# Performance work log

Measured on AMD Instinct MI355X. Metric: run time of the kernel, lower is better.

The kernel has to match this reference:

```python
import jax, jax.numpy as jnp
import numpy as np

B, T, NEMBD, NVOCAB, HID = 32, 64, 64, 256, 4096


def setup_inputs() -> dict:
    key = jax.random.key(0)
    ks = jax.random.split(key, 12)
    s = 0.1  # keep activations in a sane range
    return {
        "X": jax.random.randint(ks[0], (B, T), 0, NVOCAB, dtype=jnp.int32),
        "M": jnp.ones((B, T, 1), dtype=jnp.float32),
        "S": jnp.zeros((2, B, HID), dtype=jnp.float32),
        "embd": jax.random.normal(ks[1], (NVOCAB, NEMBD), jnp.float32) * s,
        "wx": jax.random.normal(ks[2], (NEMBD, 4 * HID), jnp.float32) * s,
        "wh": jax.random.normal(ks[3], (HID, 4 * HID), jnp.float32) * s,
        "wmx": jax.random.normal(ks[4], (NEMBD, HID), jnp.float32) * s,
        "wmh": jax.random.normal(ks[5], (HID, HID), jnp.float32) * s,
        "b": jnp.zeros((4 * HID,), jnp.float32),
        "gx": jax.random.normal(ks[6], (4 * HID,), jnp.float32),
        "gh": jax.random.normal(ks[7], (4 * HID,), jnp.float32),
        "gmx": jax.random.normal(ks[8], (HID,), jnp.float32),
        "gmh": jax.random.normal(ks[9], (HID,), jnp.float32),
        "w_out": jax.random.normal(ks[10], (HID, NVOCAB), jnp.float32) * s,
        "b_out": jnp.zeros((NVOCAB,), jnp.float32),
    }


def _wn(w, g):
    # tf.nn.l2_normalize(w, dim=0) * g  (column-wise weight norm)
    return w * (g / jnp.sqrt(jnp.sum(w * w, axis=0, keepdims=True).clip(1e-12)))


def reference(X, M, S, embd, wx, wh, wmx, wmh, b, gx, gh, gmx, gmh, w_out, b_out):
    # weight-normalized rnn weights (rnn_wn=True)
    wxn, whn = _wn(wx, gx), _wn(wh, gh)
    wmxn, wmhn = _wn(wmx, gmx), _wn(wmh, gmh)

    words = embd[X]                       # [B,T,64]
    xs = jnp.swapaxes(words, 0, 1)        # [T,B,64]
    ms = jnp.swapaxes(M, 0, 1)            # [T,B,1]
    c0, h0 = S[0], S[1]                   # [B,HID] each

    def step(carry, inp):
        c, h = carry
        x, mt = inp
        m = (x @ wmxn) * (h @ wmhn)       # multiplicative intermediate
        z = x @ wxn + m @ whn + b         # [B,4*HID]
        i, f, o, u = jnp.split(z, 4, axis=1)
        i, f, o = jax.nn.sigmoid(i), jax.nn.sigmoid(f), jax.nn.sigmoid(o)
        u = jnp.tanh(u)
        ct = f * c + i * u
        ht = o * jnp.tanh(ct)
        c = ct * mt + c * (1.0 - mt)      # mask-blend state
        h = ht * mt + h * (1.0 - mt)
        return (c, h), (c, h)

    (cf, hf), (cells, hs) = jax.lax.scan(step, (c0, h0), (xs, ms))
    states = jnp.stack([cf, hf], 0)       # [2,B,HID]
    # tf.concat(hs,1) then reshape [-1,HID] => batch-major (b, t) row order
    hflat = jnp.swapaxes(hs, 0, 1).reshape(-1, hs.shape[-1])  # [B*T,HID]
    logits = hflat @ w_out + b_out        # out_wn=False
    return cells, states, logits
```

## Files before the change

### kernel.cpp

```cpp
#include <hip/hip_runtime.h>
#include <hip/hip_bf16.h>

#define HID 4096
#define NEMBD 64
#define NBATCH 32
#define NTIME 64
#define NVOCAB 256
#define G4 16384

typedef __attribute__((ext_vector_type(4))) float f32x4;
typedef __attribute__((ext_vector_type(8))) short s16x8;

__device__ __forceinline__ unsigned short f2bf(float f) {
  union { float f; unsigned u; } v; v.f = f;
  unsigned u = v.u + 0x7FFFu + ((v.u >> 16) & 1u);
  return (unsigned short)(u >> 16);
}

__device__ __forceinline__ int apoff(int b, int j) {
  return ((j >> 5) << 10) | ((b >> 4) << 9) |
         (((b & 15) | (((j >> 3) & 3) << 4)) << 3) | (j & 7);
}

__global__ void packs_k(const float* __restrict__ src, const float* __restrict__ g,
                        unsigned short* __restrict__ dst, float* __restrict__ sc,
                        int N, int Cw, int S, int nch) {
  int bid = blockIdx.x;
  int colbase = (bid & 3) * Cw + (bid >> S) * 16;
  size_t dstbase = (size_t)bid * nch * 512;
  __shared__ unsigned short tile[512];
  __shared__ float red[16][16];
  int tid = threadIdx.x;
  int col16 = tid & 15, kk = tid >> 4;
  float s = 0.f;
  for (int c = 0; c < nch; ++c) {
    float v0 = src[(size_t)(c * 32 + kk) * N + colbase + col16];
    float v1 = src[(size_t)(c * 32 + kk + 16) * N + colbase + col16];
    s += v0 * v0 + v1 * v1;
    int l0 = col16 | (((kk >> 3) & 3) << 4);
    int l1 = col16 | ((((kk + 16) >> 3) & 3) << 4);
    tile[l0 * 8 + (kk & 7)] = f2bf(v0);
    tile[l1 * 8 + (kk & 7)] = f2bf(v1);
    __syncthreads();
    if (tid < 64)
      ((s16x8*)(dst + dstbase + (size_t)c * 512))[tid] = ((s16x8*)tile)[tid];
    __syncthreads();
  }
  if (g) {
    red[kk][col16] = s;
    __syncthreads();
    if (tid < 16) {
      float tot = 0.f;
#pragma unroll
      for (int q = 0; q < 16; ++q) tot += red[q][tid];
      sc[colbase + tid] = g[colbase + tid] / sqrtf(fmaxf(tot, 1e-12f));
    }
  }
}

__global__ void xepack_k(const int* __restrict__ X, const float* __restrict__ embd,
                         unsigned short* __restrict__ xe) {
  int t = blockIdx.x;
  int tid = threadIdx.x;
  int l = tid & 63, tile = (tid >> 6) & 1, c2 = tid >> 7;
  int b = tile * 16 + (l & 15);
  int row = X[b * NTIME + t];
  int k0 = 32 * c2 + 8 * (l >> 4);
  size_t off = (size_t)t * 2048 + c2 * 1024 + tile * 512 + l * 8;
  for (int j = 0; j < 8; ++j) xe[off + j] = f2bf(embd[row * NEMBD + k0 + j]);
}

__global__ void init_k(const float* __restrict__ S, float* __restrict__ cst,
                       float* __restrict__ hst, unsigned short* __restrict__ hpk) {
  int e = blockIdx.x * 256 + threadIdx.x;
  if (e < NBATCH * HID) {
    float c = S[e], h = S[NBATCH * HID + e];
    cst[e] = c; hst[e] = h;
    int b = e >> 12, j = e & 4095;
    hpk[apoff(b, j)] = f2bf(h);
  }
}

#define MFMA(a, b, c) __builtin_amdgcn_mfma_f32_16x16x32_bf16(a, b, c, 0, 0, 0)

__global__ __launch_bounds__(1024, 4)
void ph1_k(const unsigned short* __restrict__ wmhp, const unsigned short* __restrict__ wmxp,
           const unsigned short* __restrict__ xe, const unsigned short* __restrict__ hpk,
           const float* __restrict__ scmh, const float* __restrict__ scmx,
           unsigned short* __restrict__ mpk, int t) {
  const int g = blockIdx.x;
  const int tid = threadIdx.x;
  const int w = tid >> 6, l = tid & 63;
  const int lo = l & 15, hi = l >> 4;

  __shared__ float part[16][32][16];
  __shared__ float xmS[32][16];

  const s16x8* wmh_g = (const s16x8*)(wmhp + (size_t)g * 128 * 512);
  const s16x8* wmx_g = (const s16x8*)(wmxp + (size_t)g * 2 * 512);
  const s16x8* hp = (const s16x8*)hpk;

  f32x4 a0 = {0.f, 0.f, 0.f, 0.f}, a1 = {0.f, 0.f, 0.f, 0.f};
  const int cb = w * 8;
  {
    s16x8 wbuf[4], pa[4], pb[4];
#pragma unroll
    for (int q = 0; q < 4; ++q) {
      wbuf[q] = wmh_g[(cb + q) * 64 + l];
      pa[q] = hp[(cb + q) * 128 + l];
      pb[q] = hp[(cb + q) * 128 + 64 + l];
    }
#pragma unroll
    for (int q = 0; q < 8; ++q) {
      const int r = q & 3;
      s16x8 bf = wbuf[r], af = pa[r], gf = pb[r];
      if (q < 4) {
        wbuf[r] = wmh_g[(cb + q + 4) * 64 + l];
        pa[r] = hp[(cb + q + 4) * 128 + l];
        pb[r] = hp[(cb + q + 4) * 128 + 64 + l];
      }
      a0 = MFMA(af, bf, a0);
      a1 = MFMA(gf, bf, a1);
    }
  }
#pragma unroll
  for (int r = 0; r < 4; ++r) {
    part[w][4 * hi + r][lo] = a0[r];
    part[w][16 + 4 * hi + r][lo] = a1[r];
  }
  if (w == 0) {
    f32x4 x0 = {0.f, 0.f, 0.f, 0.f}, x1 = {0.f, 0.f, 0.f, 0.f};
    const s16x8* xep = (const s16x8*)(xe + (size_t)t * 2048);
#pragma unroll
    for (int c2 = 0; c2 < 2; ++c2) {
      s16x8 bf = wmx_g[c2 * 64 + l];
      x0 = MFMA(xep[c2 * 128 + l], bf, x0);
      x1 = MFMA(xep[c2 * 128 + 64 + l], bf, x1);
    }
#pragma unroll
    for (int r = 0; r < 4; ++r) {
      xmS[4 * hi + r][lo] = x0[r];
      xmS[16 + 4 * hi + r][lo] = x1[r];
    }
  }
  __syncthreads();
  if (tid < 512) {
    const int eb = tid >> 4, c = tid & 15;
    const int ej = g * 16 + c;
    float hm = 0.f;
#pragma unroll
    for (int k = 0; k < 16; ++k) hm += part[k][eb][c];
    mpk[apoff(eb, ej)] = f2bf(xmS[eb][c] * hm * (scmh[ej] * scmx[ej]));
  }
}

__global__ __launch_bounds__(1024, 4)
void ph2_k(const unsigned short* __restrict__ whp, const unsigned short* __restrict__ wxp,
           const unsigned short* __restrict__ xe, const float* __restrict__ bias,
           const float* __restrict__ sch, const float* __restrict__ scx,
           const float* __restrict__ Mm, const unsigned short* __restrict__ mpk,
           unsigned short* __restrict__ hpk, float* __restrict__ cst,
           float* __restrict__ hst, unsigned short* __restrict__ hflat,
           float* __restrict__ out, int t) {
  const int g = blockIdx.x;
  const int tid = threadIdx.x;
  const int w = tid >> 6, l = tid & 63;
  const int lo = l & 15, hi = l >> 4;
  const int gate = w & 3, ks = w >> 2;

  __shared__ float part[16][32][16];
  __shared__ float xpart[4][32][16];

  const s16x8* wh_w = (const s16x8*)(whp + (size_t)(g * 4 + gate) * 128 * 512);
  const s16x8* wx_w = (const s16x8*)(wxp + (size_t)(g * 4 + gate) * 2 * 512);
  const s16x8* mp = (const s16x8*)mpk;

  f32x4 z0 = {0.f, 0.f, 0.f, 0.f}, z1 = {0.f, 0.f, 0.f, 0.f};
  const int cb = ks * 32;
  {
    s16x8 wbuf[4], pa[4], pb[4];
#pragma unroll
    for (int q = 0; q < 4; ++q) {
      wbuf[q] = wh_w[(cb + q) * 64 + l];
      pa[q] = mp[(cb + q) * 128 + l];
      pb[q] = mp[(cb + q) * 128 + 64 + l];
    }
#pragma unroll
    for (int q = 0; q < 32; ++q) {
      const int r = q & 3;
      s16x8 bf = wbuf[r], af = pa[r], gf = pb[r];
      if (q < 28) {
        wbuf[r] = wh_w[(cb + q + 4) * 64 + l];
        pa[r] = mp[(cb + q + 4) * 128 + l];
        pb[r] = mp[(cb + q + 4) * 128 + 64 + l];
      }
      z0 = MFMA(af, bf, z0);
      z1 = MFMA(gf, bf, z1);
    }
  }
  if (ks == 0) {
    f32x4 x0 = {0.f, 0.f, 0.f, 0.f}, x1 = {0.f, 0.f, 0.f, 0.f};
    const s16x8* xep = (const s16x8*)(xe + (size_t)t * 2048);
#pragma unroll
    for (int c2 = 0; c2 < 2; ++c2) {
      s16x8 bf = wx_w[c2 * 64 + l];
      x0 = MFMA(xep[c2 * 128 + l], bf, x0);
      x1 = MFMA(xep[c2 * 128 + 64 + l], bf, x1);
    }
#pragma unroll
    for (int r = 0; r < 4; ++r) {
      xpart[gate][4 * hi + r][lo] = x0[r];
      xpart[gate][16 + 4 * hi + r][lo] = x1[r];
    }
  }
#pragma unroll
  for (int r = 0; r < 4; ++r) {
    part[w][4 * hi + r][lo] = z0[r];
    part[w][16 + 4 * hi + r][lo] = z1[r];
  }
  __syncthreads();
  if (tid < 512) {
    const int eb = tid >> 4, c = tid & 15;
    const int ej = g * 16 + c;
    float zh, iv, fv, ov, uv;
    zh = part[0][eb][c] + part[4][eb][c] + part[8][eb][c] + part[12][eb][c];
    iv = zh * sch[ej] + xpart[0][eb][c] * scx[ej] + bias[ej];
    zh = part[1][eb][c] + part[5][eb][c] + part[9][eb][c] + part[13][eb][c];
    fv = zh * sch[4096 + ej] + xpart[1][eb][c] * scx[4096 + ej] + bias[4096 + ej];
    zh = part[2][eb][c] + part[6][eb][c] + part[10][eb][c] + part[14][eb][c];
    ov = zh * sch[8192 + ej] + xpart[2][eb][c] * scx[8192 + ej] + bias[8192 + ej];
    zh = part[3][eb][c] + part[7][eb][c] + part[11][eb][c] + part[15][eb][c];
    uv = zh * sch[12288 + ej] + xpart[3][eb][c] * scx[12288 + ej] + bias[12288 + ej];
    iv = 1.f / (1.f + __expf(-iv));
    fv = 1.f / (1.f + __expf(-fv));
    ov = 1.f / (1.f + __expf(-ov));
    uv = tanhf(uv);
    size_t sj = (size_t)eb * HID + ej;
    float cp = cst[sj], hpv = hst[sj];
    float ct = fv * cp + iv * uv;
    float ht = ov * tanhf(ct);
    float mt = Mm[eb * NTIME + t];
    float cn = ct * mt + cp * (1.f - mt);
    float hn = ht * mt + hpv * (1.f - mt);
    cst[sj] = cn;
    hst[sj] = hn;
    out[((size_t)t * NBATCH + eb) * HID + ej] = cn;
    unsigned short hb = f2bf(hn);
    {
      int tle = eb * 4 + (t >> 4);
      int r16 = t & 15;
      int kk2 = ej & 31;
      int lane2 = r16 | (((kk2 >> 3) & 3) << 4);
      hflat[(size_t)tle * 65536 + (size_t)(ej >> 5) * 512 + lane2 * 8 + (kk2 & 7)] = hb;
    }
    hpk[apoff(eb, ej)] = hb;
    if (t == NTIME - 1) {
      out[(size_t)NTIME * NBATCH * HID + sj] = cn;
      out[(size_t)NTIME * NBATCH * HID + NBATCH * HID + sj] = hn;
    }
  }
}

__global__ __launch_bounds__(256)
void logits_k(const unsigned short* __restrict__ hpA,
              const unsigned short* __restrict__ woutp,
              const float* __restrict__ bout, float* __restrict__ out) {
  int tle = blockIdx.x >> 1, ch = blockIdx.x & 1;
  int tid = threadIdx.x, w = tid >> 6, l = tid & 63;
  int lo = l & 15, hi = l >> 4;
  const s16x8* ap = (const s16x8*)(hpA + (size_t)tle * 65536);
  const s16x8* wp = (const s16x8*)woutp;
  f32x4 acc[2] = {{0.f,0.f,0.f,0.f},{0.f,0.f,0.f,0.f}};
  const int nt0 = ch * 8 + w * 2;
#pragma unroll 4
  for (int c = 0; c < 128; ++c) {
    s16x8 af = ap[c * 64 + l];
    acc[0] = MFMA(af, wp[((nt0 + 0) * 128 + c) * 64 + l], acc[0]);
    acc[1] = MFMA(af, wp[((nt0 + 1) * 128 + c) * 64 + l], acc[1]);
  }
  int r0 = tle * 16;
#pragma unroll
  for (int q = 0; q < 2; ++q) {
    int col = (nt0 + q) * 16 + lo;
    float bo = bout[col];
#pragma unroll
    for (int r = 0; r < 4; ++r)
      out[(size_t)(r0 + 4 * hi + r) * NVOCAB + col] = acc[q][r] + bo;
  }
}

extern "C" void kernel_launch(void* const* d_in, const int* in_sizes, int n_in,
                              void* d_out, int out_size, void* d_ws, size_t ws_size,
                              hipStream_t stream) {
  const int*   X    = (const int*)d_in[0];
  const float* Mm   = (const float*)d_in[1];
  const float* S    = (const float*)d_in[2];
  const float* embd = (const float*)d_in[3];
  const float* wx   = (const float*)d_in[4];
  const float* wh   = (const float*)d_in[5];
  const float* wmx  = (const float*)d_in[6];
  const float* wmh  = (const float*)d_in[7];
  const float* b    = (const float*)d_in[8];
  const float* gx   = (const float*)d_in[9];
  const float* gh   = (const float*)d_in[10];
  const float* gmx  = (const float*)d_in[11];
  const float* gmh  = (const float*)d_in[12];
  const float* wout = (const float*)d_in[13];
  const float* bout = (const float*)d_in[14];
  float* out = (float*)d_out;
  char* ws = (char*)d_ws;

  size_t cur = 0;
  auto alloc = [&](size_t bytes) { size_t o = cur; cur += (bytes + 255) & ~size_t(255); return o; };
  unsigned short* WHP   = (unsigned short*)(ws + alloc((size_t)1024 * 128 * 512 * 2));
  unsigned short* WMHP  = (unsigned short*)(ws + alloc((size_t)256 * 128 * 512 * 2));
  unsigned short* WXP   = (unsigned short*)(ws + alloc((size_t)1024 * 2 * 512 * 2));
  unsigned short* WMXP  = (unsigned short*)(ws + alloc((size_t)256 * 2 * 512 * 2));
  unsigned short* WOUTP = (unsigned short*)(ws + alloc((size_t)16 * 128 * 512 * 2));
  unsigned short* XE    = (unsigned short*)(ws + alloc((size_t)64 * 2048 * 2));
  unsigned short* MPK   = (unsigned short*)(ws + alloc((size_t)32 * 4096 * 2));
  unsigned short* HPK   = (unsigned short*)(ws + alloc((size_t)32 * 4096 * 2));
  float* CST            = (float*)(ws + alloc((size_t)32 * 4096 * 4));
  float* HST            = (float*)(ws + alloc((size_t)32 * 4096 * 4));
  unsigned short* HFLAT = (unsigned short*)(ws + alloc((size_t)2048 * 4096 * 2));
  float* SCH            = (float*)(ws + alloc((size_t)16384 * 4));
  float* SCX            = (float*)(ws + alloc((size_t)16384 * 4));
  float* SCMH           = (float*)(ws + alloc((size_t)4096 * 4));
  float* SCMX           = (float*)(ws + alloc((size_t)4096 * 4));
  (void)ws_size; (void)in_sizes; (void)n_in; (void)out_size;

  packs_k<<<1024, 256, 0, stream>>>(wh,   gh,  WHP,   SCH,  G4,    4096, 2, 128);
  packs_k<<<256,  256, 0, stream>>>(wmh,  gmh, WMHP,  SCMH, HID,   0,    0, 128);
  packs_k<<<1024, 256, 0, stream>>>(wx,   gx,  WXP,   SCX,  G4,    4096, 2, 2);
  packs_k<<<256,  256, 0, stream>>>(wmx,  gmx, WMXP,  SCMX, HID,   0,    0, 2);
  packs_k<<<16,   256, 0, stream>>>(wout, nullptr, WOUTP, nullptr, NVOCAB, 0, 0, 128);

  xepack_k<<<64, 256, 0, stream>>>(X, embd, XE);
  init_k<<<512, 256, 0, stream>>>(S, CST, HST, HPK);

  for (int t = 0; t < NTIME; ++t) {
    ph1_k<<<256, 1024, 0, stream>>>(WMHP, WMXP, XE, HPK, SCMH, SCMX, MPK, t);
    ph2_k<<<256, 1024, 0, stream>>>(WHP, WXP, XE, b, SCH, SCX, Mm, MPK, HPK, CST, HST,
                                    HFLAT, out, t);
  }

  logits_k<<<256, 256, 0, stream>>>(HFLAT, WOUTP, bout,
                                    out + (size_t)NTIME * NBATCH * HID + 2 * NBATCH * HID);
}
```

Measured before the change: 2.414 ms.

## Widen weight-pack reads to 64 columns and deepen weight prefetch in recurrent GEMMs

The weight packing kernel now has each block handle 64 contiguous columns, so every row read is a 256-byte coalesced access instead of 64 bytes, and fewer blocks are launched. In the per-timestep phase kernels, all eight weight fragments (ph1) or an 8-deep ring of them (ph2) are now prefetched, while the activation prefetch depth drops to 2. The goal is to hide more global-load latency on the large weight stream, at the cost of extra registers and possibly lower occupancy.

```diff
diff --git a/kernel.cpp b/kernel.cpp
--- a/kernel.cpp
+++ b/kernel.cpp
@@ -22,38 +22,39 @@
          (((b & 15) | (((j >> 3) & 3) << 4)) << 3) | (j & 7);
 }
 
-__global__ void packs_k(const float* __restrict__ src, const float* __restrict__ g,
-                        unsigned short* __restrict__ dst, float* __restrict__ sc,
-                        int N, int Cw, int S, int nch) {
-  int bid = blockIdx.x;
-  int colbase = (bid & 3) * Cw + (bid >> S) * 16;
-  size_t dstbase = (size_t)bid * nch * 512;
-  __shared__ unsigned short tile[512];
-  __shared__ float red[16][16];
-  int tid = threadIdx.x;
-  int col16 = tid & 15, kk = tid >> 4;
+__global__ void packs64_k(const float* __restrict__ src, const float* __restrict__ g,
+                          unsigned short* __restrict__ dst, float* __restrict__ sc,
+                          int N, int nch, int four) {
+  const int c0 = blockIdx.x * 64;
+  const int tid = threadIdx.x;
+  const int cl = tid & 63, kr = tid >> 6;
+  const int c = c0 + cl;
+  __shared__ unsigned short tile4[4][512];
+  __shared__ float red[4][64];
+  const int wti = tid >> 6;
+  const int wcol = c0 + wti * 16;
+  const int wtile = four ? ((((wcol & 4095) >> 4) << 2) | (wcol >> 12)) : (wcol >> 4);
+  unsigned short* wdst = dst + (size_t)wtile * nch * 512;
   float s = 0.f;
-  for (int c = 0; c < nch; ++c) {
-    float v0 = src[(size_t)(c * 32 + kk) * N + colbase + col16];
-    float v1 = src[(size_t)(c * 32 + kk + 16) * N + colbase + col16];
-    s += v0 * v0 + v1 * v1;
-    int l0 = col16 | (((kk >> 3) & 3) << 4);
-    int l1 = col16 | ((((kk + 16) >> 3) & 3) << 4);
-    tile[l0 * 8 + (kk & 7)] = f2bf(v0);
-    tile[l1 * 8 + (kk & 7)] = f2bf(v1);
+  const int ti = cl >> 4, col16 = cl & 15;
+  for (int ch = 0; ch < nch; ++ch) {
+#pragma unroll
+    for (int sub = 0; sub < 8; ++sub) {
+      int k32 = kr * 8 + sub;
+      float v = src[(size_t)(ch * 32 + k32) * N + c];
+      s += v * v;
+      tile4[ti][(col16 | (kr << 4)) * 8 + sub] = f2bf(v);
+    }
     __syncthreads();
-    if (tid < 64)
-      ((s16x8*)(dst + dstbase + (size_t)c * 512))[tid] = ((s16x8*)tile)[tid];
+    ((s16x8*)(wdst + (size_t)ch * 512))[tid & 63] = ((s16x8*)tile4[wti])[tid & 63];
     __syncthreads();
   }
   if (g) {
-    red[kk][col16] = s;
+    red[kr][cl] = s;
     __syncthreads();
-    if (tid < 16) {
-      float tot = 0.f;
-#pragma unroll
-      for (int q = 0; q < 16; ++q) tot += red[q][tid];
-      sc[colbase + tid] = g[colbase + tid] / sqrtf(fmaxf(tot, 1e-12f));
+    if (tid < 64) {
+      float tot = red[0][cl] + red[1][cl] + red[2][cl] + red[3][cl];
+      sc[c0 + cl] = g[c0 + cl] / sqrtf(fmaxf(tot, 1e-12f));
     }
   }
 }
@@ -103,21 +104,21 @@
   f32x4 a0 = {0.f, 0.f, 0.f, 0.f}, a1 = {0.f, 0.f, 0.f, 0.f};
   const int cb = w * 8;
   {
-    s16x8 wbuf[4], pa[4], pb[4];
-#pragma unroll
-    for (int q = 0; q < 4; ++q) {
-      wbuf[q] = wmh_g[(cb + q) * 64 + l];
+    s16x8 wbuf[8], pa[2], pb[2];
+#pragma unroll
+    for (int q = 0; q < 8; ++q) wbuf[q] = wmh_g[(cb + q) * 64 + l];
+#pragma unroll
+    for (int q = 0; q < 2; ++q) {
       pa[q] = hp[(cb + q) * 128 + l];
       pb[q] = hp[(cb + q) * 128 + 64 + l];
     }
 #pragma unroll
     for (int q = 0; q < 8; ++q) {
-      const int r = q & 3;
-      s16x8 bf = wbuf[r], af = pa[r], gf = pb[r];
-      if (q < 4) {
-        wbuf[r] = wmh_g[(cb + q + 4) * 64 + l];
-        pa[r] = hp[(cb + q + 4) * 128 + l];
-        pb[r] = hp[(cb + q + 4) * 128 + 64 + l];
+      const int r2 = q & 1;
+      s16x8 bf = wbuf[q], af = pa[r2], gf = pb[r2];
+      if (q < 6) {
+        pa[r2] = hp[(cb + q + 2) * 128 + l];
+        pb[r2] = hp[(cb + q + 2) * 128 + 64 + l];
       }
       a0 = MFMA(af, bf, a0);
       a1 = MFMA(gf, bf, a1);
@@ -178,21 +179,22 @@
   f32x4 z0 = {0.f, 0.f, 0.f, 0.f}, z1 = {0.f, 0.f, 0.f, 0.f};
   const int cb = ks * 32;
   {
-    s16x8 wbuf[4], pa[4], pb[4];
-#pragma unroll
-    for (int q = 0; q < 4; ++q) {
-      wbuf[q] = wh_w[(cb + q) * 64 + l];
+    s16x8 wbuf[8], pa[2], pb[2];
+#pragma unroll
+    for (int q = 0; q < 8; ++q) wbuf[q] = wh_w[(cb + q) * 64 + l];
+#pragma unroll
+    for (int q = 0; q < 2; ++q) {
       pa[q] = mp[(cb + q) * 128 + l];
       pb[q] = mp[(cb + q) * 128 + 64 + l];
     }
 #pragma unroll
     for (int q = 0; q < 32; ++q) {
-      const int r = q & 3;
-      s16x8 bf = wbuf[r], af = pa[r], gf = pb[r];
-      if (q < 28) {
-        wbuf[r] = wh_w[(cb + q + 4) * 64 + l];
-        pa[r] = mp[(cb + q + 4) * 128 + l];
-        pb[r] = mp[(cb + q + 4) * 128 + 64 + l];
+      const int r8 = q & 7, r2 = q & 1;
+      s16x8 bf = wbuf[r8], af = pa[r2], gf = pb[r2];
+      if (q < 24) wbuf[r8] = wh_w[(cb + q + 8) * 64 + l];
+      if (q < 30) {
+        pa[r2] = mp[(cb + q + 2) * 128 + l];
+        pb[r2] = mp[(cb + q + 2) * 128 + 64 + l];
       }
       z0 = MFMA(af, bf, z0);
       z1 = MFMA(gf, bf, z1);
@@ -329,11 +331,11 @@
   float* SCMX           = (float*)(ws + alloc((size_t)4096 * 4));
   (void)ws_size; (void)in_sizes; (void)n_in; (void)out_size;
 
-  packs_k<<<1024, 256, 0, stream>>>(wh,   gh,  WHP,   SCH,  G4,    4096, 2, 128);
-  packs_k<<<256,  256, 0, stream>>>(wmh,  gmh, WMHP,  SCMH, HID,   0,    0, 128);
-  packs_k<<<1024, 256, 0, stream>>>(wx,   gx,  WXP,   SCX,  G4,    4096, 2, 2);
-  packs_k<<<256,  256, 0, stream>>>(wmx,  gmx, WMXP,  SCMX, HID,   0,    0, 2);
-  packs_k<<<16,   256, 0, stream>>>(wout, nullptr, WOUTP, nullptr, NVOCAB, 0, 0, 128);
+  packs64_k<<<256, 256, 0, stream>>>(wh,   gh,  WHP,   SCH,  G4,    128, 1);
+  packs64_k<<<64,  256, 0, stream>>>(wmh,  gmh, WMHP,  SCMH, HID,   128, 0);
+  packs64_k<<<256, 256, 0, stream>>>(wx,   gx,  WXP,   SCX,  G4,    2,   1);
+  packs64_k<<<64,  256, 0, stream>>>(wmx,  gmx, WMXP,  SCMX, HID,   2,   0);
+  packs64_k<<<4,   256, 0, stream>>>(wout, nullptr, WOUTP, nullptr, NVOCAB, 128, 0);
 
   xepack_k<<<64, 256, 0, stream>>>(X, embd, XE);
   init_k<<<512, 256, 0, stream>>>(S, CST, HST, HPK);
```

New measurement: 2.552 ms. +5.7%, slower.
